# Kernel tuning notes

Measured on AMD Instinct MI355X. Metric: run time of the kernel, lower is better.

Reference implementation:

```python
import jax, jax.numpy as jnp
import numpy as np

NV, NE = 2048, 8192
IN_V, OUT_V, IN_E = 128, 128, 128


def setup_inputs() -> dict:
    key = jax.random.key(0)
    ks = jax.random.split(key, 8)
    stdv = 1.0 / np.sqrt(OUT_V)
    return {
        "H_v": jax.random.normal(ks[0], (NV, IN_V), jnp.float32),
        "H_e": jax.random.normal(ks[1], (NE, IN_E), jnp.float32),
        "adj_e": jax.random.uniform(ks[2], (NE, NE), jnp.float32),
        "adj_v": jax.random.uniform(ks[3], (NV, NV), jnp.float32),
        "T": jax.random.uniform(ks[4], (NV, NE), jnp.float32),
        "weight": jax.random.uniform(ks[5], (IN_V, OUT_V), jnp.float32, -stdv, stdv),
        "p": jax.random.normal(ks[6], (1, IN_E), jnp.float32),
        "bias": jax.random.uniform(ks[7], (OUT_V,), jnp.float32, -stdv, stdv),
    }


def reference(H_v, H_e, adj_e, adj_v, T, weight, p, bias):
    # node_layer=True branch.
    # edge scalar weights: diag(H_e @ p^T) -> just a vector of length NE
    w = (H_e @ p.T)[:, 0]                      # [NE]
    # T @ diag(w) @ T^T == (T * w) @ T^T  (column-scale then GEMM)
    multiplier1 = (T * w[None, :]) @ T.T       # [NV, NV]
    eye = jnp.eye(multiplier1.shape[0], dtype=multiplier1.dtype)
    M1 = eye + (1.0 - eye) * multiplier1       # ones on diag, multiplier1 off-diag
    adjusted_A = M1 * adj_v                    # masked adjacency
    ret = adjusted_A @ (H_v @ weight) + bias   # [NV, OUT_V]
    return (ret, H_e)
```

## Files before the change

kernel.cpp:

```cpp
#include <hip/hip_runtime.h>
#include <hip/hip_bf16.h>
#include <stdint.h>
#include <stddef.h>

#define NV 2048
#define NE 8192
#define NSPLIT1 7
#define KSPLIT2 16
#define KCHUNK2 (NV / KSPLIT2)

typedef __bf16 bf16_t;
typedef __bf16 bf16x4 __attribute__((ext_vector_type(4)));
typedef __bf16 bf16x8 __attribute__((ext_vector_type(8)));
typedef float f32x4 __attribute__((ext_vector_type(4)));
typedef float f32x16 __attribute__((ext_vector_type(16)));

__device__ static inline void load_lds16(const void* g, void* lds) {
  __builtin_amdgcn_global_load_lds(
      (const __attribute__((address_space(1))) void*)g,
      (__attribute__((address_space(3))) void*)lds,
      16, 0, 0);
}

__device__ static inline void tile_decode(int tile, int& bi, int& bj) {
  int b = (int)((sqrtf(8.f * tile + 1.f) - 1.f) * 0.5f);
  while ((b + 1) * (b + 2) / 2 <= tile) b++;
  while (b * (b + 1) / 2 > tile) b--;
  bi = b;
  bj = tile - b * (b + 1) / 2;
}

__global__ void k_w(const float* __restrict__ He, const float* __restrict__ p,
                    float* __restrict__ w) {
  int wave = threadIdx.x >> 6;
  int lane = threadIdx.x & 63;
  int e = blockIdx.x * 4 + wave;
  float v = He[(size_t)e * 128 + lane] * p[lane]
          + He[(size_t)e * 128 + 64 + lane] * p[64 + lane];
#pragma unroll
  for (int off = 32; off > 0; off >>= 1) v += __shfl_down(v, off, 64);
  if (lane == 0) w[e] = v;
}

__global__ void k_conv(const float* __restrict__ T, const float* __restrict__ w,
                       bf16_t* __restrict__ A, bf16_t* __restrict__ B) {
  size_t idx = (size_t)blockIdx.x * 256 + threadIdx.x;
  size_t base = idx * 4;
  int col = (int)(base & (NE - 1));
  f32x4 t = *(const f32x4*)(T + base);
  f32x4 w4 = *(const f32x4*)(w + col);
  bf16x4 a, b;
  a.x = (bf16_t)(t.x * w4.x); a.y = (bf16_t)(t.y * w4.y);
  a.z = (bf16_t)(t.z * w4.z); a.w = (bf16_t)(t.w * w4.w);
  b.x = (bf16_t)t.x; b.y = (bf16_t)t.y; b.z = (bf16_t)t.z; b.w = (bf16_t)t.w;
  *(bf16x4*)(A + base) = a;
  *(bf16x4*)(B + base) = b;
}

__global__ void k_hw(const float* __restrict__ Hv, const float* __restrict__ Wt,
                     bf16_t* __restrict__ HWt) {
  int t = blockIdx.x * 256 + threadIdx.x;
  int o = t & 127, j = t >> 7;
  const float* hv = Hv + (size_t)j * 128;
  float acc = 0.f;
#pragma unroll 4
  for (int k = 0; k < 128; ++k) acc += hv[k] * Wt[k * 128 + o];
  HWt[(size_t)o * NV + j] = (bf16_t)acc;
}

__global__ void __launch_bounds__(512, 2)
k_gemm1(const bf16_t* __restrict__ A, const bf16_t* __restrict__ B,
        bf16_t* __restrict__ P) {
  __shared__ bf16_t As[256 * 64];
  __shared__ bf16_t Bs[256 * 64];
  const int t = threadIdx.x;
  const int lane = t & 63;
  const int wv = t >> 6;
  const int wm = wv >> 2, wn = wv & 3;

  int Bi, Bj;
  tile_decode(blockIdx.x, Bi, Bj);
  const int i0 = Bi * 256, j0 = Bj * 256;
  const int y = blockIdx.y;
  const int kbeg = y * 1152;
  const int kend = (y == 6) ? NE : kbeg + 1152;
  bf16_t* Mp = P + ((size_t)blockIdx.x * NSPLIT1 + y) * 65536;

  f32x16 acc[4][2] = {};

  const int lrow = t >> 3;
  const int cb = ((t & 7) + lrow) & 7;
  const bf16_t* Ag = A + (size_t)(i0 + lrow) * NE + cb * 8;
  const bf16_t* Bg = B + (size_t)(j0 + lrow) * NE + cb * 8;

  for (int k0 = kbeg; k0 < kend; k0 += 64) {
    __syncthreads();
#pragma unroll
    for (int it = 0; it < 4; ++it) {
      load_lds16(Ag + (size_t)(it * 64) * NE + k0, (char*)As + it * 8192 + t * 16);
      load_lds16(Bg + (size_t)(it * 64) * NE + k0, (char*)Bs + it * 8192 + t * 16);
    }
    __syncthreads();
#pragma unroll
    for (int kk = 0; kk < 64; kk += 16) {
      bf16x8 af[4], bfr[2];
#pragma unroll
      for (int mt = 0; mt < 4; ++mt) {
        int row = wm * 128 + mt * 32 + (lane & 31);
        int sw = (((kk >> 3) + (lane >> 5)) - row) & 7;
        af[mt] = *(const bf16x8*)&As[row * 64 + sw * 8];
      }
#pragma unroll
      for (int nt = 0; nt < 2; ++nt) {
        int row = wn * 64 + nt * 32 + (lane & 31);
        int sw = (((kk >> 3) + (lane >> 5)) - row) & 7;
        bfr[nt] = *(const bf16x8*)&Bs[row * 64 + sw * 8];
      }
#pragma unroll
      for (int mt = 0; mt < 4; ++mt)
#pragma unroll
        for (int nt = 0; nt < 2; ++nt)
          acc[mt][nt] = __builtin_amdgcn_mfma_f32_32x32x16_bf16(af[mt], bfr[nt], acc[mt][nt], 0, 0, 0);
    }
  }

#pragma unroll
  for (int mt = 0; mt < 4; ++mt) {
#pragma unroll
    for (int nt = 0; nt < 2; ++nt) {
      int tc = wn * 64 + nt * 32 + (lane & 31);
#pragma unroll
      for (int reg = 0; reg < 16; ++reg) {
        int tr = wm * 128 + mt * 32 + (reg & 3) + 8 * (reg >> 2) + 4 * (lane >> 5);
        Mp[tr * 256 + tc] = (bf16_t)acc[mt][nt][reg];
      }
    }
  }
}

__global__ void k_mask(const bf16_t* __restrict__ P, const float* __restrict__ adj_v,
                       bf16_t* __restrict__ adjA) {
  __shared__ float Ms[128 * 129];
  const int t = threadIdx.x;
  int bi, bj;
  tile_decode(blockIdx.x, bi, bj);
  const int i0 = bi * 128, j0 = bj * 128;
  const bool diag = (bi == bj);
  const int Bi = bi >> 1, Bj = bj >> 1;
  const int qa = bi & 1, qb = bj & 1;
  const int st = Bi * (Bi + 1) / 2 + Bj;
  const bf16_t* Pt = P + (size_t)st * (NSPLIT1 * 65536)
                   + (size_t)(qa * 128) * 256 + qb * 128;
#pragma unroll 2
  for (int c = 0; c < 8; ++c) {
    int e0 = (c * 256 + t) * 8;
    int r = e0 >> 7, col = e0 & 127;
    float v[8] = {};
#pragma unroll
    for (int s = 0; s < NSPLIT1; ++s) {
      bf16x8 pv = *(const bf16x8*)(Pt + (size_t)s * 65536 + r * 256 + col);
#pragma unroll
      for (int u = 0; u < 8; ++u) v[u] += (float)pv[u];
    }
    size_t g = (size_t)(i0 + r) * NV + j0 + col;
    f32x4 av0 = *(const f32x4*)(adj_v + g);
    f32x4 av1 = *(const f32x4*)(adj_v + g + 4);
    bf16x8 outv;
#pragma unroll
    for (int u = 0; u < 8; ++u) {
      float vv = (diag && r == col + u) ? 1.0f : v[u];
      outv[u] = (bf16_t)(vv * (u < 4 ? av0[u] : av1[u - 4]));
    }
    *(bf16x8*)(adjA + g) = outv;
    if (!diag) {
#pragma unroll
      for (int u = 0; u < 8; ++u) Ms[(col + u) * 129 + r] = v[u];
    }
  }
  if (diag) return;
  __syncthreads();
#pragma unroll 2
  for (int c = 0; c < 8; ++c) {
    int e0 = (c * 256 + t) * 8;
    int r = e0 >> 7, col = e0 & 127;
    size_t g = (size_t)(j0 + r) * NV + i0 + col;
    f32x4 av0 = *(const f32x4*)(adj_v + g);
    f32x4 av1 = *(const f32x4*)(adj_v + g + 4);
    bf16x8 outv;
#pragma unroll
    for (int u = 0; u < 8; ++u)
      outv[u] = (bf16_t)(Ms[r * 129 + col + u] * (u < 4 ? av0[u] : av1[u - 4]));
    *(bf16x8*)(adjA + g) = outv;
  }
}

__global__ void k_gemm2(const bf16_t* __restrict__ adjA, const bf16_t* __restrict__ HWt,
                        float* __restrict__ P2) {
  __shared__ bf16_t As[128 * 64];
  __shared__ bf16_t Bs[128 * 64];
  const int t = threadIdx.x;
  const int lane = t & 63;
  const int wv = t >> 6;
  const int wm = wv >> 1, wn = wv & 1;
  const int i0 = blockIdx.x * 128;
  const int kbeg = blockIdx.y * KCHUNK2;
  float* Pp = P2 + (size_t)blockIdx.y * (NV * 128);

  f32x4 acc[4][4] = {};

  const int lrow = t >> 3;
  const int cb = ((t & 7) + lrow) & 7;
  const bf16_t* Ag = adjA + (size_t)(i0 + lrow) * NV + cb * 8;
  const bf16_t* Bg = HWt + (size_t)lrow * NV + cb * 8;

  for (int k0 = kbeg; k0 < kbeg + KCHUNK2; k0 += 64) {
    __syncthreads();
#pragma unroll
    for (int it = 0; it < 4; ++it) {
      load_lds16(Ag + (size_t)(it * 32) * NV + k0, (char*)As + (it * 256 + t) * 16);
      load_lds16(Bg + (size_t)(it * 32) * NV + k0, (char*)Bs + (it * 256 + t) * 16);
    }
    __syncthreads();
#pragma unroll
    for (int kk = 0; kk < 64; kk += 32) {
      bf16x8 af[4], bfr[4];
#pragma unroll
      for (int mt = 0; mt < 4; ++mt) {
        int row = wm * 64 + mt * 16 + (lane & 15);
        int sw = (((kk >> 3) + (lane >> 4)) - row) & 7;
        af[mt] = *(const bf16x8*)&As[row * 64 + sw * 8];
      }
#pragma unroll
      for (int nt = 0; nt < 4; ++nt) {
        int row = wn * 64 + nt * 16 + (lane & 15);
        int sw = (((kk >> 3) + (lane >> 4)) - row) & 7;
        bfr[nt] = *(const bf16x8*)&Bs[row * 64 + sw * 8];
      }
#pragma unroll
      for (int mt = 0; mt < 4; ++mt)
#pragma unroll
        for (int nt = 0; nt < 4; ++nt)
          acc[mt][nt] = __builtin_amdgcn_mfma_f32_16x16x32_bf16(af[mt], bfr[nt], acc[mt][nt], 0, 0, 0);
    }
  }

#pragma unroll
  for (int mt = 0; mt < 4; ++mt) {
#pragma unroll
    for (int nt = 0; nt < 4; ++nt) {
      int gc = wn * 64 + nt * 16 + (lane & 15);
#pragma unroll
      for (int r = 0; r < 4; ++r) {
        int gr = i0 + wm * 64 + mt * 16 + (lane >> 4) * 4 + r;
        Pp[(size_t)gr * 128 + gc] = acc[mt][nt][r];
      }
    }
  }
}

__global__ void k_bias(const float* __restrict__ P2, const float* __restrict__ bias,
                       const float* __restrict__ He, float* __restrict__ out) {
  int b = blockIdx.x;
  if (b < 256) {
    int idx = (b * 256 + threadIdx.x) * 4;
    f32x4 acc = {};
#pragma unroll
    for (int s = 0; s < KSPLIT2; ++s)
      acc += *(const f32x4*)(P2 + (size_t)s * NV * 128 + idx);
    f32x4 bb = *(const f32x4*)(bias + (idx & 127));
    *(f32x4*)(out + idx) = acc + bb;
  } else {
    size_t idx = ((size_t)(b - 256) * 256 + threadIdx.x) * 4;
    *(f32x4*)(out + (size_t)NV * 128 + idx) = *(const f32x4*)(He + idx);
  }
}

extern "C" void kernel_launch(void* const* d_in, const int* in_sizes, int n_in,
                              void* d_out, int out_size, void* d_ws, size_t ws_size,
                              hipStream_t stream) {
  const float* Hv     = (const float*)d_in[0];
  const float* He     = (const float*)d_in[1];
  const float* adj_v  = (const float*)d_in[3];
  const float* T      = (const float*)d_in[4];
  const float* weight = (const float*)d_in[5];
  const float* p      = (const float*)d_in[6];
  const float* bias   = (const float*)d_in[7];
  float* out = (float*)d_out;

  char* ws = (char*)d_ws;
  bf16_t* A_bf  = (bf16_t*)ws;
  bf16_t* B_bf  = (bf16_t*)(ws + 33554432);
  bf16_t* P1    = (bf16_t*)(ws + 67108864);
  bf16_t* adjAb = (bf16_t*)(ws + 104857600);
  float*  P2    = (float*)(ws + 113246208);
  bf16_t* HWt   = (bf16_t*)(ws + 130023424);
  float*  w     = (float*)(ws + 130547712);

  k_w<<<NE / 4, 256, 0, stream>>>(He, p, w);
  k_conv<<<(NV * NE / 4) / 256, 256, 0, stream>>>(T, w, A_bf, B_bf);
  k_hw<<<(NV * 128) / 256, 256, 0, stream>>>(Hv, weight, HWt);
  dim3 g1(36, NSPLIT1);
  k_gemm1<<<g1, 512, 0, stream>>>(A_bf, B_bf, P1);
  k_mask<<<136, 256, 0, stream>>>(P1, adj_v, adjAb);
  dim3 g2(NV / 128, KSPLIT2);
  k_gemm2<<<g2, 256, 0, stream>>>(adjAb, HWt, P2);
  k_bias<<<256 + (NE * 128) / (4 * 256), 256, 0, stream>>>(P2, bias, He, out);
}
```

Measured before the change: 456.3 us.

## Double-buffer LDS tiles in k_gemm1 to overlap global loads with MFMA

Splits the k_gemm1 shared-memory A/B tiles into two buffers and prefetches the next K-slice into the idle buffer while MFMAs run on the current one. This cuts one barrier per iteration and is meant to hide global-to-LDS load latency. LDS use doubles to 128 KB per block, so launch bounds drop to one 512-thread block per CU, which lowers occupancy.

```diff
diff --git a/kernel.cpp b/kernel.cpp
--- a/kernel.cpp
+++ b/kernel.cpp
@@ -68,11 +68,11 @@
   HWt[(size_t)o * NV + j] = (bf16_t)acc;
 }
 
-__global__ void __launch_bounds__(512, 2)
+__global__ void __launch_bounds__(512, 1)
 k_gemm1(const bf16_t* __restrict__ A, const bf16_t* __restrict__ B,
         bf16_t* __restrict__ P) {
-  __shared__ bf16_t As[256 * 64];
-  __shared__ bf16_t Bs[256 * 64];
+  __shared__ bf16_t As[2][256 * 64];
+  __shared__ bf16_t Bs[2][256 * 64];
   const int t = threadIdx.x;
   const int lane = t & 63;
   const int wv = t >> 6;
@@ -93,14 +93,25 @@
   const bf16_t* Ag = A + (size_t)(i0 + lrow) * NE + cb * 8;
   const bf16_t* Bg = B + (size_t)(j0 + lrow) * NE + cb * 8;
 
+#define STAGE1(buf, kk0)                                                     \
+  do {                                                                       \
+    _Pragma("unroll")                                                        \
+    for (int it = 0; it < 4; ++it) {                                         \
+      load_lds16(Ag + (size_t)(it * 64) * NE + (kk0),                        \
+                 (char*)As[buf] + it * 8192 + t * 16);                       \
+      load_lds16(Bg + (size_t)(it * 64) * NE + (kk0),                        \
+                 (char*)Bs[buf] + it * 8192 + t * 16);                       \
+    }                                                                        \
+  } while (0)
+
+  STAGE1(0, kbeg);
+  __syncthreads();
+  int cur = 0;
+
   for (int k0 = kbeg; k0 < kend; k0 += 64) {
-    __syncthreads();
-#pragma unroll
-    for (int it = 0; it < 4; ++it) {
-      load_lds16(Ag + (size_t)(it * 64) * NE + k0, (char*)As + it * 8192 + t * 16);
-      load_lds16(Bg + (size_t)(it * 64) * NE + k0, (char*)Bs + it * 8192 + t * 16);
-    }
-    __syncthreads();
+    if (k0 + 64 < kend) STAGE1(cur ^ 1, k0 + 64);
+    const bf16_t* Asr = As[cur];
+    const bf16_t* Bsr = Bs[cur];
 #pragma unroll
     for (int kk = 0; kk < 64; kk += 16) {
       bf16x8 af[4], bfr[2];
@@ -108,13 +119,13 @@
       for (int mt = 0; mt < 4; ++mt) {
         int row = wm * 128 + mt * 32 + (lane & 31);
         int sw = (((kk >> 3) + (lane >> 5)) - row) & 7;
-        af[mt] = *(const bf16x8*)&As[row * 64 + sw * 8];
+        af[mt] = *(const bf16x8*)&Asr[row * 64 + sw * 8];
       }
 #pragma unroll
       for (int nt = 0; nt < 2; ++nt) {
         int row = wn * 64 + nt * 32 + (lane & 31);
         int sw = (((kk >> 3) + (lane >> 5)) - row) & 7;
-        bfr[nt] = *(const bf16x8*)&Bs[row * 64 + sw * 8];
+        bfr[nt] = *(const bf16x8*)&Bsr[row * 64 + sw * 8];
       }
 #pragma unroll
       for (int mt = 0; mt < 4; ++mt)
@@ -122,7 +133,10 @@
         for (int nt = 0; nt < 2; ++nt)
           acc[mt][nt] = __builtin_amdgcn_mfma_f32_32x32x16_bf16(af[mt], bfr[nt], acc[mt][nt], 0, 0, 0);
     }
-  }
+    __syncthreads();
+    cur ^= 1;
+  }
+#undef STAGE1
 
 #pragma unroll
   for (int mt = 0; mt < 4; ++mt) {
```

Result: no change. 450.4 us (-1.3%).
